# Kernel optimization log

Measured on AMD Instinct MI355X. Metric: run time of the kernel, lower is better.

Reference implementation:

```python
import jax, jax.numpy as jnp
import numpy as np

B, N, D = 4, 2048, 1024
HEADS, DIM_HEAD = 16, 64
INNER = HEADS * DIM_HEAD  # 1024
SCALE = DIM_HEAD ** -0.5


def setup_inputs() -> dict:
    key = jax.random.key(0)
    ks = jax.random.split(key, 8)
    w = 0.02
    return {
        "x":  jax.random.normal(ks[0], (B, N, D), dtype=jnp.float32),
        "Wq": jax.random.normal(ks[1], (D, INNER), dtype=jnp.float32) * w,
        "bq": jax.random.normal(ks[2], (INNER,), dtype=jnp.float32) * w,
        "Wv": jax.random.normal(ks[3], (D, INNER), dtype=jnp.float32) * w,
        "bv": jax.random.normal(ks[4], (INNER,), dtype=jnp.float32) * w,
        "Wo": jax.random.normal(ks[5], (INNER, D), dtype=jnp.float32) * w,
        "bo": jax.random.normal(ks[6], (D,), dtype=jnp.float32) * w,
    }


def reference(x, Wq, bq, Wv, bv, Wo, bo):
    b, n, _ = x.shape
    q = x @ Wq + bq                      # [b, n, inner]
    v = x @ Wv + bv                      # [b, n, inner]
    # split heads -> [b, h, n, d]
    q = q.reshape(b, n, HEADS, DIM_HEAD).transpose(0, 2, 1, 3).astype(jnp.float32)
    v = v.reshape(b, n, HEADS, DIM_HEAD).transpose(0, 2, 1, 3)
    # k = q (self L2 attention)
    AB = jnp.einsum('bhid,bhjd->bhij', q, q)          # [b, h, n, n]
    AA = jnp.sum(q * q, axis=-1, keepdims=True)       # [b, h, n, 1]
    BB = jnp.swapaxes(AA, -1, -2)                     # [b, h, 1, n]
    sim = -(AA - 2.0 * AB + BB) * SCALE               # negative scaled L2 distance
    attn = jax.nn.softmax(sim, axis=-1)
    out = jnp.einsum('bhij,bhjd->bhid', attn, v)      # [b, h, n, d]
    out = out.transpose(0, 2, 1, 3).reshape(b, n, INNER)
    return out @ Wo + bo
```

## Files before the change

kernel.cpp:

```cpp
#include <hip/hip_runtime.h>
#include <hip/hip_bf16.h>

#define SEQ 2048
#define SCALE 0.125f
#define LOG2E 1.4426950408889634f

typedef __bf16 bf16;
typedef __bf16 bf16x4 __attribute__((ext_vector_type(4)));
typedef __bf16 bf16x8 __attribute__((ext_vector_type(8)));
typedef _Float16 f16;
typedef _Float16 f16x2 __attribute__((ext_vector_type(2)));
typedef _Float16 f16x4 __attribute__((ext_vector_type(4)));
typedef float f32x4 __attribute__((ext_vector_type(4)));
typedef unsigned int u32;
typedef unsigned int u32x4 __attribute__((ext_vector_type(4)));

__device__ __forceinline__ f16x2 pk_f16(float a, float b) {
    return __builtin_bit_cast(f16x2, __builtin_amdgcn_cvt_pkrtz(a, b));
}

__device__ __forceinline__ void gl_lds16(const void* g, void* l) {
    __builtin_amdgcn_global_load_lds((const __attribute__((address_space(1))) u32*)g,
                                     (__attribute__((address_space(3))) u32*)l, 16, 0, 0);
}


__global__ __launch_bounds__(256) void k_cast_x(const float4* __restrict__ x,
                                                bf16x4* __restrict__ xb) {
    int t = blockIdx.x * 256 + threadIdx.x;
    float4 f = x[t];
    bf16x4 o;
    o[0] = (bf16)f.x; o[1] = (bf16)f.y; o[2] = (bf16)f.z; o[3] = (bf16)f.w;
    xb[t] = o;
}

__global__ __launch_bounds__(256) void k_transpose_cast(const float* __restrict__ src,
                                                        bf16* __restrict__ dst) {
    __shared__ float tile[32][33];
    int bx = blockIdx.x * 32;
    int by = blockIdx.y * 32;
    int tx = threadIdx.x;
    int ty = threadIdx.y;
#pragma unroll
    for (int j = 0; j < 32; j += 8)
        tile[ty + j][tx] = src[(size_t)(by + ty + j) * 1024 + bx + tx];
    __syncthreads();
#pragma unroll
    for (int j = 0; j < 32; j += 8)
        dst[(size_t)(bx + ty + j) * 1024 + by + tx] = (bf16)tile[tx][ty + j];
}


__global__ __launch_bounds__(256) void k_gemm_qv(const bf16* __restrict__ Xb,
                                                 const bf16* __restrict__ Wqvt,
                                                 const float* __restrict__ bq,
                                                 const float* __restrict__ bv,
                                                 bf16* __restrict__ Q,
                                                 f16* __restrict__ Vt,
                                                 float* __restrict__ QN) {
    constexpr int K = 1024;
    __shared__ bf16 As[128 * 32];
    __shared__ bf16 Bs[128 * 32];
    int t = threadIdx.x, w = t >> 6, l = t & 63;
    int blockN = blockIdx.x * 128, blockM = blockIdx.y * 128;
    int wm = w & 1, wn = w >> 1;
    int lr = l & 15, quad = l >> 4, q8 = quad * 8;
    int skcol = (l & 3) * 8;
    bool isQ = blockN < 1024;

    f32x4 acc[4][4] = {};
    const bf16* Ab = Xb + (size_t)blockM * K;
    const bf16* Bb = Wqvt + (size_t)blockN * K;

    for (int k0 = 0; k0 < K; k0 += 32) {
#pragma unroll
        for (int c2 = 0; c2 < 2; ++c2) {
            int c = 2 * w + c2;
            int row = c * 16 + (l >> 2);
            gl_lds16(Ab + (size_t)row * K + k0 + skcol, As + c * 512);
            gl_lds16(Bb + (size_t)row * K + k0 + skcol, Bs + c * 512);
        }
        __syncthreads();
        const bf16* Aw = As + wm * 64 * 32;
        const bf16* Bw = Bs + wn * 64 * 32;
        bf16x8 af[4], bfr[4];
#pragma unroll
        for (int mi = 0; mi < 4; ++mi) af[mi] = *(const bf16x8*)(Aw + (mi * 16 + lr) * 32 + q8);
#pragma unroll
        for (int ni = 0; ni < 4; ++ni) bfr[ni] = *(const bf16x8*)(Bw + (ni * 16 + lr) * 32 + q8);
        if (isQ) {
#pragma unroll
            for (int mi = 0; mi < 4; ++mi)
#pragma unroll
                for (int ni = 0; ni < 4; ++ni)
                    acc[mi][ni] = __builtin_amdgcn_mfma_f32_16x16x32_bf16(af[mi], bfr[ni], acc[mi][ni], 0, 0, 0);
        } else {
#pragma unroll
            for (int mi = 0; mi < 4; ++mi)
#pragma unroll
                for (int ni = 0; ni < 4; ++ni)
                    acc[mi][ni] = __builtin_amdgcn_mfma_f32_16x16x32_bf16(bfr[ni], af[mi], acc[mi][ni], 0, 0, 0);
        }
        __syncthreads();
    }

    int colbase = blockN + wn * 64;
    if (isQ) {
        int h = colbase >> 6;
        float bias[4];
#pragma unroll
        for (int ni = 0; ni < 4; ++ni) bias[ni] = bq[colbase + ni * 16 + lr];
#pragma unroll
        for (int mi = 0; mi < 4; ++mi) {
#pragma unroll
            for (int r = 0; r < 4; ++r) {
                int m = blockM + wm * 64 + mi * 16 + quad * 4 + r;
                int b = m >> 11, s = m & 2047;
                int bh = (b << 4) + h;
                float qsq = 0.f;
#pragma unroll
                for (int ni = 0; ni < 4; ++ni) {
                    float v = acc[mi][ni][r] + bias[ni];
                    bf16 vb = (bf16)v;
                    Q[((size_t)bh * SEQ + s) * 64 + ni * 16 + lr] = vb;
                    float vr = (float)vb;
                    qsq += vr * vr;
                }
                qsq += __shfl_xor(qsq, 1);
                qsq += __shfl_xor(qsq, 2);
                qsq += __shfl_xor(qsq, 4);
                qsq += __shfl_xor(qsq, 8);
                if (lr == 0) QN[(size_t)bh * SEQ + s] = qsq;
            }
        }
    } else {
        int h = (colbase - 1024) >> 6;
        int b = blockM >> 11;
        int bh = (b << 4) + h;
        int s_base = (blockM & 2047) + wm * 64;
        const float* bvh = bv + (colbase - 1024);
#pragma unroll
        for (int ni = 0; ni < 4; ++ni) {
#pragma unroll
            for (int r = 0; r < 4; ++r) {
                int dh = ni * 16 + quad * 4 + r;
                float bias = bvh[dh];
#pragma unroll
                for (int mi = 0; mi < 4; ++mi) {
                    int s = s_base + mi * 16 + lr;
                    Vt[((size_t)bh * 64 + dh) * SEQ + s] = (f16)(acc[mi][ni][r] + bias);
                }
            }
        }
    }
}


__global__ __launch_bounds__(256, 4) void k_attn(const bf16* __restrict__ Q,
                                                 const f16* __restrict__ Vt,
                                                 const float* __restrict__ QN,
                                                 bf16* __restrict__ AO) {
    __shared__ bf16 Ks[64 * 64];
    __shared__ f16 Vs[64 * 72];
    __shared__ float BBl[2048];
    __shared__ float Dl[4][32];

    int t = threadIdx.x, w = t >> 6, l = t & 63;
    int bh = blockIdx.y;
    int i0 = blockIdx.x * 128;
    const bf16* Qh = Q + (size_t)bh * SEQ * 64;
    const f16* Vh = Vt + (size_t)bh * 64 * SEQ;
    int lr = l & 15, quad = l >> 4, q8 = quad * 8, lr7 = lr & 7;

    {
        const float4* QN4 = (const float4*)(QN + (size_t)bh * SEQ);
        float4* BB4 = (float4*)BBl;
#pragma unroll
        for (int i = 0; i < 2; ++i) {
            float4 v = QN4[t + i * 256];
            v.x *= (SCALE * LOG2E); v.y *= (SCALE * LOG2E);
            v.z *= (SCALE * LOG2E); v.w *= (SCALE * LOG2E);
            BB4[t + i * 256] = v;
        }
    }

    bf16x8 af[2][2];
#pragma unroll
    for (int mi = 0; mi < 2; ++mi)
#pragma unroll
        for (int kc = 0; kc < 2; ++kc)
            af[mi][kc] = *(const bf16x8*)(Qh + (size_t)(i0 + w * 32 + mi * 16 + lr) * 64 + kc * 32 + q8);

    f32x4 oacc[2][4] = {};
    float dpart[2] = {0.f, 0.f};

    int kb[2];
#pragma unroll
    for (int kc = 0; kc < 2; ++kc) kb[kc] = lr * 64 + (((kc * 4 + quad) ^ lr7) * 8);
    int vb[4];
#pragma unroll
    for (int di = 0; di < 4; ++di) vb[di] = (di * 16 + lr) * 72 + quad * 4;

    int sr0 = t >> 3, sc0 = t & 7;
    int sr1 = sr0 + 32;
    int ksl0 = sr0 * 64 + ((sc0 ^ (sr0 & 7)) * 8);
    int ksl1 = sr1 * 64 + ((sc0 ^ (sr1 & 7)) * 8);
    int vsl0 = sr0 * 72 + sc0 * 8;
    int vsl1 = sr1 * 72 + sc0 * 8;

    u32x4 rk0 = *(const u32x4*)(Qh + (size_t)sr0 * 64 + sc0 * 8);
    u32x4 rk1 = *(const u32x4*)(Qh + (size_t)sr1 * 64 + sc0 * 8);
    u32x4 rv0 = *(const u32x4*)(Vh + (size_t)sr0 * SEQ + sc0 * 8);
    u32x4 rv1 = *(const u32x4*)(Vh + (size_t)sr1 * SEQ + sc0 * 8);

    const float c2s = 2.f * SCALE * LOG2E;

    for (int j0 = 0; j0 < SEQ; j0 += 64) {
        __syncthreads();
        *(u32x4*)(Ks + ksl0) = rk0;
        *(u32x4*)(Ks + ksl1) = rk1;
        *(u32x4*)(Vs + vsl0) = rv0;
        *(u32x4*)(Vs + vsl1) = rv1;
        int jn = j0 + 64;
        if (jn < SEQ) {
            rk0 = *(const u32x4*)(Qh + (size_t)(jn + sr0) * 64 + sc0 * 8);
            rk1 = *(const u32x4*)(Qh + (size_t)(jn + sr1) * 64 + sc0 * 8);
            rv0 = *(const u32x4*)(Vh + (size_t)sr0 * SEQ + jn + sc0 * 8);
            rv1 = *(const u32x4*)(Vh + (size_t)sr1 * SEQ + jn + sc0 * 8);
        }
        __syncthreads();

#pragma unroll
        for (int ni = 0; ni < 4; ++ni) {
            bf16x8 bk0 = *(const bf16x8*)(Ks + ni * 1024 + kb[0]);
            bf16x8 bk1 = *(const bf16x8*)(Ks + ni * 1024 + kb[1]);
            f32x4 sT0 = {}, sT1 = {};
            sT0 = __builtin_amdgcn_mfma_f32_16x16x32_bf16(bk0, af[0][0], sT0, 0, 0, 0);
            sT0 = __builtin_amdgcn_mfma_f32_16x16x32_bf16(bk1, af[0][1], sT0, 0, 0, 0);
            sT1 = __builtin_amdgcn_mfma_f32_16x16x32_bf16(bk0, af[1][0], sT1, 0, 0, 0);
            sT1 = __builtin_amdgcn_mfma_f32_16x16x32_bf16(bk1, af[1][1], sT1, 0, 0, 0);

            f32x4 bbt = *(const f32x4*)(BBl + j0 + ni * 16 + quad * 4);

            float p00 = __builtin_amdgcn_exp2f(sT0[0] * c2s - bbt[0]);
            float p01 = __builtin_amdgcn_exp2f(sT0[1] * c2s - bbt[1]);
            float p02 = __builtin_amdgcn_exp2f(sT0[2] * c2s - bbt[2]);
            float p03 = __builtin_amdgcn_exp2f(sT0[3] * c2s - bbt[3]);
            float p10 = __builtin_amdgcn_exp2f(sT1[0] * c2s - bbt[0]);
            float p11 = __builtin_amdgcn_exp2f(sT1[1] * c2s - bbt[1]);
            float p12 = __builtin_amdgcn_exp2f(sT1[2] * c2s - bbt[2]);
            float p13 = __builtin_amdgcn_exp2f(sT1[3] * c2s - bbt[3]);
            dpart[0] += (p00 + p01) + (p02 + p03);
            dpart[1] += (p10 + p11) + (p12 + p13);

            f16x2 a0 = pk_f16(p00, p01);
            f16x2 a1 = pk_f16(p02, p03);
            f16x2 b0 = pk_f16(p10, p11);
            f16x2 b1 = pk_f16(p12, p13);
            f16x4 pf0 = {a0[0], a0[1], a1[0], a1[1]};
            f16x4 pf1 = {b0[0], b0[1], b1[0], b1[1]};

#pragma unroll
            for (int di = 0; di < 4; ++di) {
                f16x4 vf = *(const f16x4*)(Vs + vb[di] + ni * 16);
                oacc[0][di] = __builtin_amdgcn_mfma_f32_16x16x16f16(pf0, vf, oacc[0][di], 0, 0, 0);
                oacc[1][di] = __builtin_amdgcn_mfma_f32_16x16x16f16(pf1, vf, oacc[1][di], 0, 0, 0);
            }
        }
    }

#pragma unroll
    for (int mi = 0; mi < 2; ++mi) {
        float ds = dpart[mi];
        ds += __shfl_xor(ds, 16);
        ds += __shfl_xor(ds, 32);
        if (quad == 0) Dl[w][mi * 16 + lr] = ds;
    }
    __syncthreads();

    int b = bh >> 4, h = bh & 15;
#pragma unroll
    for (int mi = 0; mi < 2; ++mi) {
#pragma unroll
        for (int r = 0; r < 4; ++r) {
            float inv = 1.f / Dl[w][mi * 16 + quad * 4 + r];
            int s = i0 + w * 32 + mi * 16 + quad * 4 + r;
#pragma unroll
            for (int di = 0; di < 4; ++di) {
                AO[((size_t)(b * SEQ + s)) * 1024 + h * 64 + di * 16 + lr] = (bf16)(oacc[mi][di][r] * inv);
            }
        }
    }
}


__global__ __launch_bounds__(256) void k_gemm_out(const bf16* __restrict__ AO,
                                                  const bf16* __restrict__ Wot,
                                                  const float* __restrict__ bo,
                                                  float* __restrict__ out) {
    constexpr int K = 1024;
    __shared__ bf16 As[128 * 32];
    __shared__ bf16 Bs[128 * 32];
    int t = threadIdx.x, w = t >> 6, l = t & 63;
    int blockN = blockIdx.x * 128, blockM = blockIdx.y * 128;
    int wm = w & 1, wn = w >> 1;
    int lr = l & 15, quad = l >> 4, q8 = quad * 8;
    int skcol = (l & 3) * 8;

    f32x4 acc[4][4] = {};
    const bf16* Ab = AO + (size_t)blockM * K;
    const bf16* Bb = Wot + (size_t)blockN * K;

    for (int k0 = 0; k0 < K; k0 += 32) {
#pragma unroll
        for (int c2 = 0; c2 < 2; ++c2) {
            int c = 2 * w + c2;
            int row = c * 16 + (l >> 2);
            gl_lds16(Ab + (size_t)row * K + k0 + skcol, As + c * 512);
            gl_lds16(Bb + (size_t)row * K + k0 + skcol, Bs + c * 512);
        }
        __syncthreads();
        const bf16* Aw = As + wm * 64 * 32;
        const bf16* Bw = Bs + wn * 64 * 32;
        bf16x8 af[4], bfr[4];
#pragma unroll
        for (int mi = 0; mi < 4; ++mi) af[mi] = *(const bf16x8*)(Aw + (mi * 16 + lr) * 32 + q8);
#pragma unroll
        for (int ni = 0; ni < 4; ++ni) bfr[ni] = *(const bf16x8*)(Bw + (ni * 16 + lr) * 32 + q8);
#pragma unroll
        for (int mi = 0; mi < 4; ++mi)
#pragma unroll
            for (int ni = 0; ni < 4; ++ni)
                acc[mi][ni] = __builtin_amdgcn_mfma_f32_16x16x32_bf16(af[mi], bfr[ni], acc[mi][ni], 0, 0, 0);
        __syncthreads();
    }

    int colbase = blockN + wn * 64;
    float bias[4];
#pragma unroll
    for (int ni = 0; ni < 4; ++ni) bias[ni] = bo[colbase + ni * 16 + lr];
#pragma unroll
    for (int mi = 0; mi < 4; ++mi) {
#pragma unroll
        for (int r = 0; r < 4; ++r) {
            int m = blockM + wm * 64 + mi * 16 + quad * 4 + r;
#pragma unroll
            for (int ni = 0; ni < 4; ++ni) {
                out[(size_t)m * 1024 + colbase + ni * 16 + lr] = acc[mi][ni][r] + bias[ni];
            }
        }
    }
}


extern "C" void kernel_launch(void* const* d_in, const int* in_sizes, int n_in,
                              void* d_out, int out_size, void* d_ws, size_t ws_size,
                              hipStream_t stream) {
    const float* x  = (const float*)d_in[0];
    const float* Wq = (const float*)d_in[1];
    const float* bq = (const float*)d_in[2];
    const float* Wv = (const float*)d_in[3];
    const float* bv = (const float*)d_in[4];
    const float* Wo = (const float*)d_in[5];
    const float* bo = (const float*)d_in[6];
    float* out = (float*)d_out;

    char* ws = (char*)d_ws;
    bf16* Xb   = (bf16*)ws;
    bf16* Wqvt = (bf16*)(ws + (size_t)(16 << 20));
    bf16* Wot  = (bf16*)(ws + (size_t)(20 << 20));
    bf16* Qb   = (bf16*)(ws + (size_t)(22 << 20));
    f16*  Vtb  = (f16*)(ws + (size_t)(38 << 20));
    float* QN  = (float*)(ws + (size_t)(54 << 20));
    bf16* AO   = Xb;

    k_cast_x<<<8192, 256, 0, stream>>>((const float4*)x, (bf16x4*)Xb);
    dim3 tb(32, 8);
    k_transpose_cast<<<dim3(32, 32), tb, 0, stream>>>(Wq, Wqvt);
    k_transpose_cast<<<dim3(32, 32), tb, 0, stream>>>(Wv, Wqvt + 1024 * 1024);
    k_transpose_cast<<<dim3(32, 32), tb, 0, stream>>>(Wo, Wot);
    k_gemm_qv<<<dim3(16, 64), 256, 0, stream>>>(Xb, Wqvt, bq, bv, Qb, Vtb, QN);
    k_attn<<<dim3(16, 64), 256, 0, stream>>>(Qb, Vtb, QN, AO);
    k_gemm_out<<<dim3(8, 64), 256, 0, stream>>>(AO, Wot, bo, out);
}
```

Baseline: 307.0 us.

## Fold softmax scale into Q, bias into MFMA init, rowsum via MFMA

```diff
diff --git a/kernel.cpp b/kernel.cpp
--- a/kernel.cpp
+++ b/kernel.cpp
@@ -4,6 +4,7 @@
 #define SEQ 2048
 #define SCALE 0.125f
 #define LOG2E 1.4426950408889634f
+#define ALPHA 0.6005612049f
 
 typedef __bf16 bf16;
 typedef __bf16 bf16x4 __attribute__((ext_vector_type(4)));
@@ -11,8 +12,10 @@
 typedef _Float16 f16;
 typedef _Float16 f16x2 __attribute__((ext_vector_type(2)));
 typedef _Float16 f16x4 __attribute__((ext_vector_type(4)));
+typedef _Float16 f16x8 __attribute__((ext_vector_type(8)));
 typedef float f32x4 __attribute__((ext_vector_type(4)));
 typedef unsigned int u32;
+typedef unsigned int u32x2 __attribute__((ext_vector_type(2)));
 typedef unsigned int u32x4 __attribute__((ext_vector_type(4)));
 
 __device__ __forceinline__ f16x2 pk_f16(float a, float b) {
@@ -120,7 +123,7 @@
                 float qsq = 0.f;
 #pragma unroll
                 for (int ni = 0; ni < 4; ++ni) {
-                    float v = acc[mi][ni][r] + bias[ni];
+                    float v = (acc[mi][ni][r] + bias[ni]) * ALPHA;
                     bf16 vb = (bf16)v;
                     Q[((size_t)bh * SEQ + s) * 64 + ni * 16 + lr] = vb;
                     float vr = (float)vb;
@@ -130,7 +133,7 @@
                 qsq += __shfl_xor(qsq, 2);
                 qsq += __shfl_xor(qsq, 4);
                 qsq += __shfl_xor(qsq, 8);
-                if (lr == 0) QN[(size_t)bh * SEQ + s] = qsq;
+                if (lr == 0) QN[(size_t)bh * SEQ + s] = -0.5f * qsq;
             }
         }
     } else {
@@ -161,9 +164,8 @@
                                                  const float* __restrict__ QN,
                                                  bf16* __restrict__ AO) {
     __shared__ bf16 Ks[64 * 64];
-    __shared__ f16 Vs[64 * 72];
+    __shared__ f16 Vs[64 * 64];
     __shared__ float BBl[2048];
-    __shared__ float Dl[4][32];
 
     int t = threadIdx.x, w = t >> 6, l = t & 63;
     int bh = blockIdx.y;
@@ -175,13 +177,8 @@
     {
         const float4* QN4 = (const float4*)(QN + (size_t)bh * SEQ);
         float4* BB4 = (float4*)BBl;
-#pragma unroll
-        for (int i = 0; i < 2; ++i) {
-            float4 v = QN4[t + i * 256];
-            v.x *= (SCALE * LOG2E); v.y *= (SCALE * LOG2E);
-            v.z *= (SCALE * LOG2E); v.w *= (SCALE * LOG2E);
-            BB4[t + i * 256] = v;
-        }
+        BB4[t] = QN4[t];
+        BB4[t + 256] = QN4[t + 256];
     }
 
     bf16x8 af[2][2];
@@ -192,98 +189,109 @@
             af[mi][kc] = *(const bf16x8*)(Qh + (size_t)(i0 + w * 32 + mi * 16 + lr) * 64 + kc * 32 + q8);
 
     f32x4 oacc[2][4] = {};
-    float dpart[2] = {0.f, 0.f};
+    f32x4 dacc[2] = {};
+    const f16x4 ones = {(f16)1.f, (f16)1.f, (f16)1.f, (f16)1.f};
 
     int kb[2];
 #pragma unroll
     for (int kc = 0; kc < 2; ++kc) kb[kc] = lr * 64 + (((kc * 4 + quad) ^ lr7) * 8);
-    int vb[4];
-#pragma unroll
-    for (int di = 0; di < 4; ++di) vb[di] = (di * 16 + lr) * 72 + quad * 4;
-
-    int sr0 = t >> 3, sc0 = t & 7;
+    int voff[4];
+#pragma unroll
+    for (int di = 0; di < 4; ++di) voff[di] = (di * 16 + lr) * 64;
+    int npo[2];
+#pragma unroll
+    for (int np = 0; np < 2; ++np) npo[np] = ((np * 4 + quad) ^ lr7) * 8;
+
+    int sr0 = t >> 3, sc = t & 7;
     int sr1 = sr0 + 32;
-    int ksl0 = sr0 * 64 + ((sc0 ^ (sr0 & 7)) * 8);
-    int ksl1 = sr1 * 64 + ((sc0 ^ (sr1 & 7)) * 8);
-    int vsl0 = sr0 * 72 + sc0 * 8;
-    int vsl1 = sr1 * 72 + sc0 * 8;
-
-    u32x4 rk0 = *(const u32x4*)(Qh + (size_t)sr0 * 64 + sc0 * 8);
-    u32x4 rk1 = *(const u32x4*)(Qh + (size_t)sr1 * 64 + sc0 * 8);
-    u32x4 rv0 = *(const u32x4*)(Vh + (size_t)sr0 * SEQ + sc0 * 8);
-    u32x4 rv1 = *(const u32x4*)(Vh + (size_t)sr1 * SEQ + sc0 * 8);
-
-    const float c2s = 2.f * SCALE * LOG2E;
+    int ksl0 = sr0 * 64 + ((sc ^ (sr0 & 7)) * 8);
+    int ksl1 = sr1 * 64 + ((sc ^ (sr1 & 7)) * 8);
+    int np_s = sc >> 2, ni1_s = (sc >> 1) & 1, q0_s = (sc & 1) * 2;
+    int cpA = np_s * 4 + q0_s, cpB = cpA + 1;
+    int vdA0 = sr0 * 64 + ((cpA ^ (sr0 & 7)) * 8) + ni1_s * 4;
+    int vdB0 = sr0 * 64 + ((cpB ^ (sr0 & 7)) * 8) + ni1_s * 4;
+    int vdA1 = sr1 * 64 + ((cpA ^ (sr1 & 7)) * 8) + ni1_s * 4;
+    int vdB1 = sr1 * 64 + ((cpB ^ (sr1 & 7)) * 8) + ni1_s * 4;
+
+    u32x4 rk0 = *(const u32x4*)(Qh + (size_t)sr0 * 64 + sc * 8);
+    u32x4 rk1 = *(const u32x4*)(Qh + (size_t)sr1 * 64 + sc * 8);
+    u32x4 rv0 = *(const u32x4*)(Vh + (size_t)sr0 * SEQ + sc * 8);
+    u32x4 rv1 = *(const u32x4*)(Vh + (size_t)sr1 * SEQ + sc * 8);
 
     for (int j0 = 0; j0 < SEQ; j0 += 64) {
         __syncthreads();
         *(u32x4*)(Ks + ksl0) = rk0;
         *(u32x4*)(Ks + ksl1) = rk1;
-        *(u32x4*)(Vs + vsl0) = rv0;
-        *(u32x4*)(Vs + vsl1) = rv1;
+        {
+            u32x2 lo0 = {rv0[0], rv0[1]}, hi0 = {rv0[2], rv0[3]};
+            u32x2 lo1 = {rv1[0], rv1[1]}, hi1 = {rv1[2], rv1[3]};
+            *(u32x2*)(Vs + vdA0) = lo0;
+            *(u32x2*)(Vs + vdB0) = hi0;
+            *(u32x2*)(Vs + vdA1) = lo1;
+            *(u32x2*)(Vs + vdB1) = hi1;
+        }
         int jn = j0 + 64;
         if (jn < SEQ) {
-            rk0 = *(const u32x4*)(Qh + (size_t)(jn + sr0) * 64 + sc0 * 8);
-            rk1 = *(const u32x4*)(Qh + (size_t)(jn + sr1) * 64 + sc0 * 8);
-            rv0 = *(const u32x4*)(Vh + (size_t)sr0 * SEQ + jn + sc0 * 8);
-            rv1 = *(const u32x4*)(Vh + (size_t)sr1 * SEQ + jn + sc0 * 8);
-        }
-        __syncthreads();
-
-#pragma unroll
-        for (int ni = 0; ni < 4; ++ni) {
-            bf16x8 bk0 = *(const bf16x8*)(Ks + ni * 1024 + kb[0]);
-            bf16x8 bk1 = *(const bf16x8*)(Ks + ni * 1024 + kb[1]);
-            f32x4 sT0 = {}, sT1 = {};
-            sT0 = __builtin_amdgcn_mfma_f32_16x16x32_bf16(bk0, af[0][0], sT0, 0, 0, 0);
-            sT0 = __builtin_amdgcn_mfma_f32_16x16x32_bf16(bk1, af[0][1], sT0, 0, 0, 0);
-            sT1 = __builtin_amdgcn_mfma_f32_16x16x32_bf16(bk0, af[1][0], sT1, 0, 0, 0);
-            sT1 = __builtin_amdgcn_mfma_f32_16x16x32_bf16(bk1, af[1][1], sT1, 0, 0, 0);
-
-            f32x4 bbt = *(const f32x4*)(BBl + j0 + ni * 16 + quad * 4);
-
-            float p00 = __builtin_amdgcn_exp2f(sT0[0] * c2s - bbt[0]);
-            float p01 = __builtin_amdgcn_exp2f(sT0[1] * c2s - bbt[1]);
-            float p02 = __builtin_amdgcn_exp2f(sT0[2] * c2s - bbt[2]);
-            float p03 = __builtin_amdgcn_exp2f(sT0[3] * c2s - bbt[3]);
-            float p10 = __builtin_amdgcn_exp2f(sT1[0] * c2s - bbt[0]);
-            float p11 = __builtin_amdgcn_exp2f(sT1[1] * c2s - bbt[1]);
-            float p12 = __builtin_amdgcn_exp2f(sT1[2] * c2s - bbt[2]);
-            float p13 = __builtin_amdgcn_exp2f(sT1[3] * c2s - bbt[3]);
-            dpart[0] += (p00 + p01) + (p02 + p03);
-            dpart[1] += (p10 + p11) + (p12 + p13);
-
-            f16x2 a0 = pk_f16(p00, p01);
-            f16x2 a1 = pk_f16(p02, p03);
-            f16x2 b0 = pk_f16(p10, p11);
-            f16x2 b1 = pk_f16(p12, p13);
-            f16x4 pf0 = {a0[0], a0[1], a1[0], a1[1]};
-            f16x4 pf1 = {b0[0], b0[1], b1[0], b1[1]};
-
+            rk0 = *(const u32x4*)(Qh + (size_t)(jn + sr0) * 64 + sc * 8);
+            rk1 = *(const u32x4*)(Qh + (size_t)(jn + sr1) * 64 + sc * 8);
+            rv0 = *(const u32x4*)(Vh + (size_t)sr0 * SEQ + jn + sc * 8);
+            rv1 = *(const u32x4*)(Vh + (size_t)sr1 * SEQ + jn + sc * 8);
+        }
+        __syncthreads();
+
+#pragma unroll
+        for (int np = 0; np < 2; ++np) {
+            f16x4 pf[2][2];
+#pragma unroll
+            for (int ni1 = 0; ni1 < 2; ++ni1) {
+                int ni = np * 2 + ni1;
+                bf16x8 bk0 = *(const bf16x8*)(Ks + ni * 1024 + kb[0]);
+                bf16x8 bk1 = *(const bf16x8*)(Ks + ni * 1024 + kb[1]);
+                f32x4 bbt = *(const f32x4*)(BBl + j0 + ni * 16 + quad * 4);
+                f32x4 sT0 = bbt, sT1 = bbt;
+                sT0 = __builtin_amdgcn_mfma_f32_16x16x32_bf16(bk0, af[0][0], sT0, 0, 0, 0);
+                sT0 = __builtin_amdgcn_mfma_f32_16x16x32_bf16(bk1, af[0][1], sT0, 0, 0, 0);
+                sT1 = __builtin_amdgcn_mfma_f32_16x16x32_bf16(bk0, af[1][0], sT1, 0, 0, 0);
+                sT1 = __builtin_amdgcn_mfma_f32_16x16x32_bf16(bk1, af[1][1], sT1, 0, 0, 0);
+
+                float p00 = __builtin_amdgcn_exp2f(sT0[0]);
+                float p01 = __builtin_amdgcn_exp2f(sT0[1]);
+                float p02 = __builtin_amdgcn_exp2f(sT0[2]);
+                float p03 = __builtin_amdgcn_exp2f(sT0[3]);
+                float p10 = __builtin_amdgcn_exp2f(sT1[0]);
+                float p11 = __builtin_amdgcn_exp2f(sT1[1]);
+                float p12 = __builtin_amdgcn_exp2f(sT1[2]);
+                float p13 = __builtin_amdgcn_exp2f(sT1[3]);
+
+                f16x2 a0 = pk_f16(p00, p01);
+                f16x2 a1 = pk_f16(p02, p03);
+                f16x2 b0 = pk_f16(p10, p11);
+                f16x2 b1 = pk_f16(p12, p13);
+                pf[0][ni1] = f16x4{a0[0], a0[1], a1[0], a1[1]};
+                pf[1][ni1] = f16x4{b0[0], b0[1], b1[0], b1[1]};
+
+                dacc[0] = __builtin_amdgcn_mfma_f32_16x16x16f16(pf[0][ni1], ones, dacc[0], 0, 0, 0);
+                dacc[1] = __builtin_amdgcn_mfma_f32_16x16x16f16(pf[1][ni1], ones, dacc[1], 0, 0, 0);
+            }
 #pragma unroll
             for (int di = 0; di < 4; ++di) {
-                f16x4 vf = *(const f16x4*)(Vs + vb[di] + ni * 16);
-                oacc[0][di] = __builtin_amdgcn_mfma_f32_16x16x16f16(pf0, vf, oacc[0][di], 0, 0, 0);
-                oacc[1][di] = __builtin_amdgcn_mfma_f32_16x16x16f16(pf1, vf, oacc[1][di], 0, 0, 0);
-            }
-        }
-    }
-
+                f16x8 vf8 = *(const f16x8*)(Vs + voff[di] + npo[np]);
+                f16x4 vlo = __builtin_shufflevector(vf8, vf8, 0, 1, 2, 3);
+                f16x4 vhi = __builtin_shufflevector(vf8, vf8, 4, 5, 6, 7);
+                oacc[0][di] = __builtin_amdgcn_mfma_f32_16x16x16f16(pf[0][0], vlo, oacc[0][di], 0, 0, 0);
+                oacc[1][di] = __builtin_amdgcn_mfma_f32_16x16x16f16(pf[1][0], vlo, oacc[1][di], 0, 0, 0);
+                oacc[0][di] = __builtin_amdgcn_mfma_f32_16x16x16f16(pf[0][1], vhi, oacc[0][di], 0, 0, 0);
+                oacc[1][di] = __builtin_amdgcn_mfma_f32_16x16x16f16(pf[1][1], vhi, oacc[1][di], 0, 0, 0);
+            }
+        }
+    }
+
+    int b = bh >> 4, h = bh & 15;
 #pragma unroll
     for (int mi = 0; mi < 2; ++mi) {
-        float ds = dpart[mi];
-        ds += __shfl_xor(ds, 16);
-        ds += __shfl_xor(ds, 32);
-        if (quad == 0) Dl[w][mi * 16 + lr] = ds;
-    }
-    __syncthreads();
-
-    int b = bh >> 4, h = bh & 15;
-#pragma unroll
-    for (int mi = 0; mi < 2; ++mi) {
 #pragma unroll
         for (int r = 0; r < 4; ++r) {
-            float inv = 1.f / Dl[w][mi * 16 + quad * 4 + r];
+            float inv = 1.f / dacc[mi][r];
             int s = i0 + w * 32 + mi * 16 + quad * 4 + r;
 #pragma unroll
             for (int di = 0; di < 4; ++di) {
```

Result: faster. 290.4 us (-5.4%).
